# Optimization experiments

Measured on AMD Instinct MI355X. Metric: run time of the kernel, lower is better.

Reference implementation:

```python
import jax, jax.numpy as jnp
import numpy as np

NUM_CAPS_OUT = 10
NUM_NODES = 32 * 6 * 6  # 1152
IN_DIM = 8
OUT_DIM = 16
ROUTING_ITERS = 3


def squash(x):
    # scale = |x|^2/(1+|x|^2); out = scale * x/|x|  (no epsilon, faithful to torch)
    sn = jnp.sum(x * x, axis=-1, keepdims=True)
    return sn / (1.0 + sn) * x / jnp.sqrt(sn)


def setup_inputs() -> dict:
    key = jax.random.key(0)
    ks = jax.random.split(key, 6)
    B = 512
    images = jax.random.normal(ks[0], (B, 1, 28, 28), dtype=jnp.float32)
    # ConvLayer: Conv2d(1, 256, k=9, s=1) with bias
    conv1_w = jax.random.normal(ks[1], (256, 1, 9, 9), dtype=jnp.float32) * 0.05
    conv1_b = jnp.zeros((256,), dtype=jnp.float32)
    prim_w = jax.random.normal(ks[2], (8 * 32, 256, 9, 9), dtype=jnp.float32) * 0.01
    prim_b = jnp.zeros((8 * 32,), dtype=jnp.float32)
    # DigitCaps weight: torch.randn(10, 1152, 8, 16)
    W = jax.random.normal(ks[3], (NUM_CAPS_OUT, NUM_NODES, IN_DIM, OUT_DIM), dtype=jnp.float32)
    return {"images": images, "conv1_w": conv1_w, "conv1_b": conv1_b,
            "prim_w": prim_w, "prim_b": prim_b, "W": W}


def reference(images, conv1_w, conv1_b, prim_w, prim_b, W):
    B = images.shape[0]
    dn = ('NCHW', 'OIHW', 'NCHW')
    # ConvLayer: 28x28 -> 20x20, 256 channels, ReLU
    x = jax.lax.conv_general_dilated(images, conv1_w, (1, 1), 'VALID', dimension_numbers=dn)
    x = jax.nn.relu(x + conv1_b[None, :, None, None])  # [B,256,20,20]
    # PrimaryCaps: 8 stacked convs -> [B, 8*32, 6, 6]; each capsule viewed as (32*6*6,)
    u = jax.lax.conv_general_dilated(x, prim_w, (2, 2), 'VALID', dimension_numbers=dn)
    u = u + prim_b[None, :, None, None]
    u = u.reshape(B, 8, NUM_NODES).transpose(0, 2, 1)  # [B,1152,8]
    u = squash(u)
    # DigitCaps: u_hat[c,b,n,o] = sum_i u[b,n,i] * W[c,n,i,o]
    u_hat = jnp.einsum('bni,cnio->cbno', u, W)  # [10,B,1152,16]
    # Dynamic routing (3 iterations). b_ij kept as [...,1]: torch replicates it
    # across the 16 out dims identically, so math is unchanged.
    b_ij = jnp.zeros(u_hat.shape[:-1] + (1,), dtype=u_hat.dtype)
    v_j = None
    for it in range(ROUTING_ITERS):
        c_ij = jax.nn.softmax(b_ij, axis=2)            # softmax over nodes
        s_j = jnp.sum(c_ij * u_hat, axis=2, keepdims=True)  # [10,B,1,16]
        v_j = squash(s_j)
        if it < ROUTING_ITERS - 1:
            a_ij = jnp.sum(u_hat * v_j, axis=-1, keepdims=True)  # [10,B,1152,1]
            b_ij = b_ij + a_ij
    # squeeze -> [10,B,16], transpose(0,1) -> [B,10,16]
    return v_j[:, :, 0, :].transpose(1, 0, 2)
```

## Files before the change

### kernel.cpp

```cpp
#include <hip/hip_runtime.h>
#include <hip/hip_bf16.h>
#include <cstddef>
#include <cstdint>

typedef __attribute__((ext_vector_type(8))) short v8s;
typedef __attribute__((ext_vector_type(16))) float v16f;

#define GLDS(SRC, DST) __builtin_amdgcn_global_load_lds( \
    (const __attribute__((address_space(1))) void*)(SRC), \
    (__attribute__((address_space(3))) void*)(DST), 16, 0, 0)

#define WAIT_VM4() asm volatile("s_waitcnt vmcnt(4)" ::: "memory")
#define WAIT_VM0() asm volatile("s_waitcnt vmcnt(0)" ::: "memory")
#define SCHED0()   __builtin_amdgcn_sched_barrier(0)

__device__ __forceinline__ void bf16split(float x, unsigned short& h, unsigned short& l) {
    union { float f; unsigned u; } a; a.f = x;
    unsigned r = a.u + 0x7fff + ((a.u >> 16) & 1);
    h = (unsigned short)(r >> 16);
    union { unsigned u; float f; } hb; hb.u = (unsigned)h << 16;
    union { float f; unsigned u; } b; b.f = x - hb.f;
    unsigned r2 = b.u + 0x7fff + ((b.u >> 16) & 1);
    l = (unsigned short)(r2 >> 16);
}

__global__ __launch_bounds__(256) void prep_kernel(
    const float* __restrict__ cw, const float* __restrict__ pw,
    float* __restrict__ wT1, char* __restrict__ wpk)
{
    int idx = blockIdx.x * 256 + threadIdx.x;
    if (idx < 81 * 256) {
        int k = idx >> 8, oc = idx & 255;
        wT1[idx] = cw[oc * 81 + k];
    }
    int Q = idx & 2047;
    int slab = idx >> 11;
    int D = Q << 4;
    int R = D >> 9;
    int v = (D & 511) ^ ((R & 31) << 4);
    int h = v >> 7, pl = (v >> 6) & 1, icb = v & 63;
    int ch = h * 64 + R;
    int g = slab / 81, k = slab - g * 81;
    int ic0 = g * 32 + (icb >> 1);
    const float* src = pw + ((size_t)ch * 256 + ic0) * 81 + k;
    v8s ov;
#pragma unroll
    for (int j = 0; j < 8; ++j) {
        unsigned short hh, ll; bf16split(src[(size_t)j * 81], hh, ll);
        ov[j] = (short)(pl ? ll : hh);
    }
    *(v8s*)(wpk + (size_t)slab * 32768 + D) = ov;
}

__global__ __launch_bounds__(256) void conv1_kernel(
    const float* __restrict__ img,
    const float* __restrict__ wT1,
    const float* __restrict__ bias,
    char* __restrict__ xc2,
    int b0)
{
    const int bl = blockIdx.x;
    const int oc = threadIdx.x;
    __shared__ __align__(16) float im[784];
    const float* ib = img + (size_t)(b0 + bl) * 784;
    for (int e = oc; e < 784; e += 256) im[e] = ib[e];
    float w[81];
#pragma unroll
    for (int k = 0; k < 81; ++k) w[k] = wT1[k * 256 + oc];
    float bv = bias[oc];
    __syncthreads();
    char* ob = xc2 + (size_t)bl * 409600;
    for (int oy = 0; oy < 20; ++oy) {
        float a[20];
#pragma unroll
        for (int ox = 0; ox < 20; ++ox) a[ox] = bv;
        for (int ky = 0; ky < 9; ++ky) {
            const float* rp = &im[(oy + ky) * 28];
            float r[28];
#pragma unroll
            for (int q = 0; q < 7; ++q) {
                float4 v4 = *(const float4*)(rp + q * 4);
                r[q * 4] = v4.x; r[q * 4 + 1] = v4.y;
                r[q * 4 + 2] = v4.z; r[q * 4 + 3] = v4.w;
            }
#pragma unroll
            for (int kx = 0; kx < 9; ++kx) {
                float wv = w[ky * 9 + kx];
#pragma unroll
                for (int ox = 0; ox < 20; ++ox)
                    a[ox] = fmaf(wv, r[ox + kx], a[ox]);
            }
        }
#pragma unroll
        for (int ox = 0; ox < 20; ++ox) {
            float av = fmaxf(a[ox], 0.f);
            unsigned short h, l; bf16split(av, h, l);
            char* rp2 = ob + (size_t)(oy * 20 + ox) * 1024;
            *(unsigned short*)(rp2 + oc * 2) = h;
            *(unsigned short*)(rp2 + 512 + oc * 2) = l;
        }
    }
}

__global__ __launch_bounds__(512, 1) void gemm_kernel(
    const char* __restrict__ xc2,
    const char* __restrict__ wpk,
    float* __restrict__ prim,
    int M, int Mtiles, int gm0)
{
    __shared__ __align__(128) char As[2][24576];
    __shared__ __align__(128) char Bs[3][32768];
    const int tid = threadIdx.x;
    const int w = tid >> 6, lane = tid & 63;
    const int wm = w & 1, wn = w >> 1;
    const int col = lane & 31, kg = lane >> 5;
    const int id = blockIdx.x;
    const int g = id / Mtiles;
    const int tile = id - g * Mtiles;
    const int m0 = tile * 192;

    int pbase[3], asrc[3];
#pragma unroll
    for (int i = 0; i < 3; ++i) {
        int d = (w * 3 + i) * 1024 + lane * 16;
        int R = d >> 9;
        int v = (d & 511) ^ ((R & 31) << 4);
        int h = v >> 7, pl = (v >> 6) & 1, icb = v & 63;
        int m = m0 + 48 * h + R; if (m >= M) m = M - 1;
        int b = m / 36, s6 = m - b * 36;
        pbase[i] = b * 400 + (s6 / 6) * 40 + (s6 % 6) * 2;
        asrc[i] = pl * 512 + g * 64 + icb;
    }
    int Abase[3], Ahof[3], Axor[3];
#pragma unroll
    for (int fm = 0; fm < 3; ++fm) {
        int m = wm * 96 + fm * 32 + col;
        int h = m / 48, R = m - h * 48;
        Abase[fm] = R * 512;
        Ahof[fm] = h * 128;
        Axor[fm] = (R & 31) << 4;
    }
    const char* wg = wpk + (size_t)g * 81 * 32768;

    v16f acc[3][2];
#pragma unroll
    for (int i = 0; i < 3; ++i)
#pragma unroll
        for (int j = 0; j < 2; ++j)
#pragma unroll
            for (int e = 0; e < 16; ++e) acc[i][j][e] = 0.f;

    auto gldsA = [&](int nb, int kk, int i) {
        const int koff = (kk / 9) * 20 + (kk % 9);
        GLDS(xc2 + (size_t)(pbase[i] + koff) * 1024 + asrc[i],
             &As[nb][(w * 3 + i) * 1024]);
    };
    auto gldsB = [&](int nb, int kk, int i) {
        GLDS(wg + (size_t)kk * 32768 + (w * 4 + i) * 1024 + lane * 16,
             &Bs[nb][(w * 4 + i) * 1024]);
    };

#pragma unroll
    for (int i = 0; i < 3; ++i) gldsA(0, 0, i);
#pragma unroll
    for (int i = 0; i < 4; ++i) gldsB(0, 0, i);
#pragma unroll
    for (int i = 0; i < 4; ++i) gldsB(1, 1, i);
    WAIT_VM4(); SCHED0();
    __builtin_amdgcn_s_barrier(); SCHED0();

    const int xr = col << 4;
    for (int k = 0; k < 81; ++k) {
        const char* Ab = &As[k & 1][0];
        const char* Bb = &Bs[k % 3][0];
        const int nA = (k + 1) & 1, nB = (k + 2) % 3;
        const bool stA = (k < 80), stB = (k < 79);

#pragma unroll
        for (int s = 0; s < 2; ++s) {
            const int vb = s * 32 + kg * 16;
            v8s Ah[3], Al[3], Bh[2], Bl[2];
#pragma unroll
            for (int fm = 0; fm < 3; ++fm) {
                const char* ap = Ab + Abase[fm];
                Ah[fm] = *(const v8s*)(ap + ((Ahof[fm] + vb) ^ Axor[fm]));
                Al[fm] = *(const v8s*)(ap + ((Ahof[fm] + 64 + vb) ^ Axor[fm]));
            }
#pragma unroll
            for (int fn = 0; fn < 2; ++fn) {
                const char* bp = Bb + (fn * 32 + col) * 512;
                Bh[fn] = *(const v8s*)(bp + ((wn * 128 + vb) ^ xr));
                Bl[fn] = *(const v8s*)(bp + ((wn * 128 + 64 + vb) ^ xr));
            }
            if (s == 0) {
                if (stA) { gldsA(nA, k + 1, 0); gldsA(nA, k + 1, 1); gldsA(nA, k + 1, 2); }
                if (stB) gldsB(nB, k + 2, 0);
            } else {
                if (stB) { gldsB(nB, k + 2, 1); gldsB(nB, k + 2, 2); gldsB(nB, k + 2, 3); }
            }

            __builtin_amdgcn_s_barrier();
            SCHED0();
            __builtin_amdgcn_s_setprio(1);
#pragma unroll
            for (int fn = 0; fn < 2; ++fn)
#pragma unroll
                for (int fm = 0; fm < 3; ++fm) {
                    acc[fm][fn] = __builtin_amdgcn_mfma_f32_32x32x16_bf16(Al[fm], Bh[fn], acc[fm][fn], 0, 0, 0);
                    acc[fm][fn] = __builtin_amdgcn_mfma_f32_32x32x16_bf16(Ah[fm], Bl[fn], acc[fm][fn], 0, 0, 0);
                    acc[fm][fn] = __builtin_amdgcn_mfma_f32_32x32x16_bf16(Ah[fm], Bh[fn], acc[fm][fn], 0, 0, 0);
                }
            __builtin_amdgcn_s_setprio(0);
            SCHED0();
            if (s == 0) {
                __builtin_amdgcn_s_barrier();
            } else if (stA) {
                if (stB) { WAIT_VM4(); } else { WAIT_VM0(); }
                SCHED0();
                __builtin_amdgcn_s_barrier(); SCHED0();
            }
        }
    }

    float* pg = prim + (size_t)gm0 * 256;
#pragma unroll
    for (int fm = 0; fm < 3; ++fm)
#pragma unroll
        for (int fn = 0; fn < 2; ++fn) {
            int ch = wn * 64 + fn * 32 + col;
#pragma unroll
            for (int rg = 0; rg < 16; ++rg) {
                int row = (rg & 3) + 8 * (rg >> 2) + 4 * kg;
                int m = m0 + wm * 96 + fm * 32 + row;
                if (m < M) atomicAdd(&pg[(size_t)m * 256 + ch], acc[fm][fn][rg]);
            }
        }
}

__global__ __launch_bounds__(256) void prim2u_kernel(
    const float* __restrict__ prim, const float* __restrict__ pb,
    float* __restrict__ u, int M)
{
    __shared__ float p[64 * 257];
    __shared__ float bsh[256];
    const int tid = threadIdx.x;
    const int rows0 = blockIdx.x * 64;
    bsh[tid] = pb[tid];
#pragma unroll
    for (int j = 0; j < 16; ++j) {
        int e4 = j * 256 + tid;
        int row = e4 >> 6, c4 = (e4 & 63) << 2;
        int rr = rows0 + row; if (rr >= M) rr = M - 1;
        float4 a = *(const float4*)(prim + (size_t)rr * 256 + c4);
        float* pp = &p[row * 257 + c4];
        pp[0] = a.x; pp[1] = a.y; pp[2] = a.z; pp[3] = a.w;
    }
    __syncthreads();
#pragma unroll
    for (int j = 0; j < 8; ++j) {
        int idx = j * 256 + tid;
        int row = idx & 63, cc = idx >> 6;
        int m = rows0 + row;
        if (m >= M) continue;
        int b = m / 36, s = m - b * 36;
        float p8[8]; float sn = 0.f;
#pragma unroll
        for (int d = 0; d < 8; ++d) {
            float v = p[row * 257 + d * 32 + cc] + bsh[d * 32 + cc];
            p8[d] = v; sn += v * v;
        }
        float fac = sqrtf(sn) / (1.0f + sn);
        float4 o0, o1;
        o0.x = fac * p8[0]; o0.y = fac * p8[1]; o0.z = fac * p8[2]; o0.w = fac * p8[3];
        o1.x = fac * p8[4]; o1.y = fac * p8[5]; o1.z = fac * p8[6]; o1.w = fac * p8[7];
        float* up = u + ((size_t)b * 1152 + cc * 36 + s) * 8;
        *(float4*)up = o0;
        *(float4*)(up + 4) = o1;
    }
}

__global__ __launch_bounds__(512) void routing_kernel(
    const float* __restrict__ u,
    const float* __restrict__ W,
    float* __restrict__ out,
    int B, int npairs)
{
    const int id = blockIdx.x;
    const int c = id / npairs;
    const int pair = id - c * npairs;
    const int b0 = pair * 2;
    const int tid = threadIdx.x;
    __shared__ float uht[2][16][1152];
    __shared__ float bijs[2][1152];
    __shared__ float red[2][4 * 17];
    __shared__ float sred[2][17];
    __shared__ float mred[2][4];

    const float* __restrict__ Wc = W + (size_t)c * (1152 * 128);
    const int b1 = (b0 + 1 < B) ? b0 + 1 : b0;
    const float* __restrict__ ub0 = u + (size_t)b0 * 9216;
    const float* __restrict__ ub1 = u + (size_t)b1 * 9216;

    for (int n = tid; n < 1152; n += 512) {
        const float4* p0 = (const float4*)(ub0 + n * 8);
        const float4* p1 = (const float4*)(ub1 + n * 8);
        float4 a0 = p0[0], a1 = p0[1], c0 = p1[0], c1 = p1[1];
        float uu0[8] = {a0.x, a0.y, a0.z, a0.w, a1.x, a1.y, a1.z, a1.w};
        float uu1[8] = {c0.x, c0.y, c0.z, c0.w, c1.x, c1.y, c1.z, c1.w};
        float acc0[16], acc1[16];
#pragma unroll
        for (int o = 0; o < 16; ++o) { acc0[o] = 0.f; acc1[o] = 0.f; }
        const float* wn = Wc + n * 128;
#pragma unroll
        for (int i = 0; i < 8; ++i)
#pragma unroll
            for (int o = 0; o < 16; ++o) {
                float wv = wn[i * 16 + o];
                acc0[o] = fmaf(uu0[i], wv, acc0[o]);
                acc1[o] = fmaf(uu1[i], wv, acc1[o]);
            }
#pragma unroll
        for (int o = 0; o < 16; ++o) { uht[0][o][n] = acc0[o]; uht[1][o][n] = acc1[o]; }
        bijs[0][n] = 0.f; bijs[1][n] = 0.f;
    }
    __syncthreads();

    const int img = tid >> 8, t = tid & 255;
    const int wid = t >> 6, lane = t & 63;
    const float* __restrict__ UHT = &uht[img][0][0];
    float* __restrict__ bij = bijs[img];
    float* __restrict__ redi = red[img];
    float* __restrict__ sredi = sred[img];
    float* __restrict__ mredi = mred[img];

    float fac = 0.f, inv = 0.f;
    for (int it = 0; it < 3; ++it) {
        float m = -3.4e38f;
        for (int n = t; n < 1152; n += 256) m = fmaxf(m, bij[n]);
#pragma unroll
        for (int off = 32; off > 0; off >>= 1) m = fmaxf(m, __shfl_down(m, off));
        if (lane == 0) mredi[wid] = m;
        __syncthreads();
        float M = fmaxf(fmaxf(mredi[0], mredi[1]), fmaxf(mredi[2], mredi[3]));
        float se = 0.f;
        float sp[16];
#pragma unroll
        for (int o = 0; o < 16; ++o) sp[o] = 0.f;
        for (int n = t; n < 1152; n += 256) {
            float e = expf(bij[n] - M);
            se += e;
#pragma unroll
            for (int o = 0; o < 16; ++o) sp[o] = fmaf(e, UHT[o * 1152 + n], sp[o]);
        }
#pragma unroll
        for (int o = 0; o < 16; ++o)
#pragma unroll
            for (int off = 32; off > 0; off >>= 1) sp[o] += __shfl_down(sp[o], off);
#pragma unroll
        for (int off = 32; off > 0; off >>= 1) se += __shfl_down(se, off);
        if (lane == 0) {
#pragma unroll
            for (int o = 0; o < 16; ++o) redi[wid * 17 + o] = sp[o];
            redi[wid * 17 + 16] = se;
        }
        __syncthreads();
        if (t < 17)
            sredi[t] = redi[t] + redi[17 + t] + redi[34 + t] + redi[51 + t];
        __syncthreads();
        inv = 1.0f / sredi[16];
        float sn = 0.f;
        float sj[16];
#pragma unroll
        for (int o = 0; o < 16; ++o) { sj[o] = sredi[o] * inv; sn = fmaf(sj[o], sj[o], sn); }
        fac = sqrtf(sn) / (1.0f + sn);
        if (it < 2) {
            float v[16];
#pragma unroll
            for (int o = 0; o < 16; ++o) v[o] = fac * sj[o];
            for (int n = t; n < 1152; n += 256) {
                float a = 0.f;
#pragma unroll
                for (int o = 0; o < 16; ++o) a = fmaf(UHT[o * 1152 + n], v[o], a);
                bij[n] += a;
            }
        }
        __syncthreads();
    }
    if (t < 16 && b0 + img < B)
        out[((size_t)(b0 + img) * 10 + c) * 16 + t] = fac * (sredi[t] * inv);
}

extern "C" void kernel_launch(void* const* d_in, const int* in_sizes, int n_in,
                              void* d_out, int out_size, void* d_ws, size_t ws_size,
                              hipStream_t stream) {
    const float* images  = (const float*)d_in[0];
    const float* conv1_w = (const float*)d_in[1];
    const float* conv1_b = (const float*)d_in[2];
    const float* prim_w  = (const float*)d_in[3];
    const float* prim_b  = (const float*)d_in[4];
    const float* W       = (const float*)d_in[5];
    float* out = (float*)d_out;

    const int B = in_sizes[0] / 784;
    const int Mg = B * 36;
    const size_t usz = (size_t)B * 1152 * 8 * 4;
    const size_t xc2_full = (size_t)B * 409600;

    char* wsb = (char*)d_ws;
    size_t off = 0;
    float* wT1 = (float*)(wsb + off);
    off += 81 * 256 * 4;
    off = (off + 1023) & ~(size_t)1023;
    char* wpk = wsb + off;
    off += (size_t)648 * 32768;
    float* prim = (float*)(wsb + off);
    off += (size_t)Mg * 256 * 4;
    size_t rem = (ws_size > off) ? ws_size - off : 0;

    float* u;
    char* xc2base;
    int Bc;
    if (rem >= xc2_full) {
        xc2base = wsb + off;
        u = (float*)xc2base;
        Bc = B;
    } else {
        u = (float*)(wsb + off);
        off += usz;
        rem = (ws_size > off) ? ws_size - off : 0;
        xc2base = wsb + off;
        long Bcmax = (long)(rem / 409600);
        if (Bcmax < 1) Bcmax = 1;
        if (Bcmax > B) Bcmax = B;
        int nch = (int)((B + Bcmax - 1) / Bcmax);
        Bc = (B + nch - 1) / nch;
        Bc = (Bc + 15) & ~15;
        if (Bc > Bcmax) Bc = (int)(Bcmax & ~15L);
        if (Bc < 1) Bc = (int)Bcmax;
    }

    hipMemsetAsync(prim, 0, (size_t)Mg * 256 * 4, stream);
    prep_kernel<<<5184, 256, 0, stream>>>(conv1_w, prim_w, wT1, wpk);

    for (int b0 = 0; b0 < B; b0 += Bc) {
        int bc = (B - b0 < Bc) ? (B - b0) : Bc;
        conv1_kernel<<<bc, 256, 0, stream>>>(images, wT1, conv1_b, xc2base, b0);
        int M = bc * 36;
        int Mtiles = (M + 191) / 192;
        gemm_kernel<<<Mtiles * 8, 512, 0, stream>>>(xc2base, wpk, prim, M, Mtiles, b0 * 36);
    }
    prim2u_kernel<<<(Mg + 63) / 64, 256, 0, stream>>>(prim, prim_b, u, Mg);
    int npairs = (B + 1) / 2;
    routing_kernel<<<npairs * 10, 512, 0, stream>>>(u, W, out, B, npairs);
}
```

Baseline: 972.8 us.

## Keep routing u_hat in registers, one image per 256-thread block

The routing kernel now keeps each thread's u_hat rows (5 nodes × 16 outputs) and routing logits in registers instead of a large shared-memory buffer covering two images per block. Blocks become one image with 256 threads, and W loads are vectorised as float4. This removes heavy LDS use so more blocks can run per CU and LDS traffic in the routing loops disappears. In exchange, W is re-read per image rather than shared across a pair, and register pressure rises.

```diff
diff --git a/kernel.cpp b/kernel.cpp
--- a/kernel.cpp
+++ b/kernel.cpp
@@ -279,79 +279,77 @@
     }
 }
 
-__global__ __launch_bounds__(512) void routing_kernel(
+__global__ __launch_bounds__(256) void routing_kernel(
     const float* __restrict__ u,
     const float* __restrict__ W,
     float* __restrict__ out,
-    int B, int npairs)
+    int B)
 {
     const int id = blockIdx.x;
-    const int c = id / npairs;
-    const int pair = id - c * npairs;
-    const int b0 = pair * 2;
-    const int tid = threadIdx.x;
-    __shared__ float uht[2][16][1152];
-    __shared__ float bijs[2][1152];
-    __shared__ float red[2][4 * 17];
-    __shared__ float sred[2][17];
-    __shared__ float mred[2][4];
+    const int c = id / B;
+    const int b = id - c * B;
+    const int t = threadIdx.x;
+    const int wid = t >> 6, lane = t & 63;
+    __shared__ float red[4 * 17];
+    __shared__ float sred[17];
+    __shared__ float mred[4];
 
     const float* __restrict__ Wc = W + (size_t)c * (1152 * 128);
-    const int b1 = (b0 + 1 < B) ? b0 + 1 : b0;
-    const float* __restrict__ ub0 = u + (size_t)b0 * 9216;
-    const float* __restrict__ ub1 = u + (size_t)b1 * 9216;
-
-    for (int n = tid; n < 1152; n += 512) {
-        const float4* p0 = (const float4*)(ub0 + n * 8);
-        const float4* p1 = (const float4*)(ub1 + n * 8);
-        float4 a0 = p0[0], a1 = p0[1], c0 = p1[0], c1 = p1[1];
-        float uu0[8] = {a0.x, a0.y, a0.z, a0.w, a1.x, a1.y, a1.z, a1.w};
-        float uu1[8] = {c0.x, c0.y, c0.z, c0.w, c1.x, c1.y, c1.z, c1.w};
-        float acc0[16], acc1[16];
-#pragma unroll
-        for (int o = 0; o < 16; ++o) { acc0[o] = 0.f; acc1[o] = 0.f; }
-        const float* wn = Wc + n * 128;
-#pragma unroll
-        for (int i = 0; i < 8; ++i)
-#pragma unroll
-            for (int o = 0; o < 16; ++o) {
-                float wv = wn[i * 16 + o];
-                acc0[o] = fmaf(uu0[i], wv, acc0[o]);
-                acc1[o] = fmaf(uu1[i], wv, acc1[o]);
-            }
-#pragma unroll
-        for (int o = 0; o < 16; ++o) { uht[0][o][n] = acc0[o]; uht[1][o][n] = acc1[o]; }
-        bijs[0][n] = 0.f; bijs[1][n] = 0.f;
-    }
-    __syncthreads();
-
-    const int img = tid >> 8, t = tid & 255;
-    const int wid = t >> 6, lane = t & 63;
-    const float* __restrict__ UHT = &uht[img][0][0];
-    float* __restrict__ bij = bijs[img];
-    float* __restrict__ redi = red[img];
-    float* __restrict__ sredi = sred[img];
-    float* __restrict__ mredi = mred[img];
+    const float* __restrict__ ub = u + (size_t)b * 9216;
+
+    float uh[5][16];
+    float bij[5];
+#pragma unroll
+    for (int j = 0; j < 5; ++j) {
+        const int n = t + 256 * j;
+        const bool valid = (j < 4) || (t < 128);
+#pragma unroll
+        for (int o = 0; o < 16; ++o) uh[j][o] = 0.f;
+        if (valid) {
+            const float4* up = (const float4*)(ub + n * 8);
+            float4 a0 = up[0], a1 = up[1];
+            float uu[8] = {a0.x, a0.y, a0.z, a0.w, a1.x, a1.y, a1.z, a1.w};
+            const float4* w4 = (const float4*)(Wc + (size_t)n * 128);
+#pragma unroll
+            for (int i = 0; i < 8; ++i)
+#pragma unroll
+                for (int q = 0; q < 4; ++q) {
+                    float4 wv = w4[i * 4 + q];
+                    uh[j][q * 4 + 0] = fmaf(uu[i], wv.x, uh[j][q * 4 + 0]);
+                    uh[j][q * 4 + 1] = fmaf(uu[i], wv.y, uh[j][q * 4 + 1]);
+                    uh[j][q * 4 + 2] = fmaf(uu[i], wv.z, uh[j][q * 4 + 2]);
+                    uh[j][q * 4 + 3] = fmaf(uu[i], wv.w, uh[j][q * 4 + 3]);
+                }
+            bij[j] = 0.f;
+        } else {
+            bij[j] = -3.4e38f;
+        }
+    }
 
     float fac = 0.f, inv = 0.f;
     for (int it = 0; it < 3; ++it) {
-        float m = -3.4e38f;
-        for (int n = t; n < 1152; n += 256) m = fmaxf(m, bij[n]);
+        float m = bij[0];
+#pragma unroll
+        for (int j = 1; j < 5; ++j) m = fmaxf(m, bij[j]);
 #pragma unroll
         for (int off = 32; off > 0; off >>= 1) m = fmaxf(m, __shfl_down(m, off));
-        if (lane == 0) mredi[wid] = m;
+        if (lane == 0) mred[wid] = m;
         __syncthreads();
-        float M = fmaxf(fmaxf(mredi[0], mredi[1]), fmaxf(mredi[2], mredi[3]));
+        float M = fmaxf(fmaxf(mred[0], mred[1]), fmaxf(mred[2], mred[3]));
         float se = 0.f;
+        float ee[5];
         float sp[16];
 #pragma unroll
         for (int o = 0; o < 16; ++o) sp[o] = 0.f;
-        for (int n = t; n < 1152; n += 256) {
-            float e = expf(bij[n] - M);
+#pragma unroll
+        for (int j = 0; j < 5; ++j) {
+            float e = expf(bij[j] - M);
+            ee[j] = e;
             se += e;
 #pragma unroll
-            for (int o = 0; o < 16; ++o) sp[o] = fmaf(e, UHT[o * 1152 + n], sp[o]);
-        }
+            for (int o = 0; o < 16; ++o) sp[o] = fmaf(e, uh[j][o], sp[o]);
+        }
+        (void)ee;
 #pragma unroll
         for (int o = 0; o < 16; ++o)
 #pragma unroll
@@ -360,34 +358,34 @@
         for (int off = 32; off > 0; off >>= 1) se += __shfl_down(se, off);
         if (lane == 0) {
 #pragma unroll
-            for (int o = 0; o < 16; ++o) redi[wid * 17 + o] = sp[o];
-            redi[wid * 17 + 16] = se;
+            for (int o = 0; o < 16; ++o) red[wid * 17 + o] = sp[o];
+            red[wid * 17 + 16] = se;
         }
         __syncthreads();
         if (t < 17)
-            sredi[t] = redi[t] + redi[17 + t] + redi[34 + t] + redi[51 + t];
+            sred[t] = red[t] + red[17 + t] + red[34 + t] + red[51 + t];
         __syncthreads();
-        inv = 1.0f / sredi[16];
+        inv = 1.0f / sred[16];
         float sn = 0.f;
         float sj[16];
 #pragma unroll
-        for (int o = 0; o < 16; ++o) { sj[o] = sredi[o] * inv; sn = fmaf(sj[o], sj[o], sn); }
+        for (int o = 0; o < 16; ++o) { sj[o] = sred[o] * inv; sn = fmaf(sj[o], sj[o], sn); }
         fac = sqrtf(sn) / (1.0f + sn);
         if (it < 2) {
             float v[16];
 #pragma unroll
             for (int o = 0; o < 16; ++o) v[o] = fac * sj[o];
-            for (int n = t; n < 1152; n += 256) {
+#pragma unroll
+            for (int j = 0; j < 5; ++j) {
                 float a = 0.f;
 #pragma unroll
-                for (int o = 0; o < 16; ++o) a = fmaf(UHT[o * 1152 + n], v[o], a);
-                bij[n] += a;
+                for (int o = 0; o < 16; ++o) a = fmaf(uh[j][o], v[o], a);
+                bij[j] += a;
             }
         }
         __syncthreads();
     }
-    if (t < 16 && b0 + img < B)
-        out[((size_t)(b0 + img) * 10 + c) * 16 + t] = fac * (sredi[t] * inv);
+    if (t < 16) out[((size_t)b * 10 + c) * 16 + t] = fac * (sred[t] * inv);
 }
 
 extern "C" void kernel_launch(void* const* d_in, const int* in_sizes, int n_in,
@@ -450,6 +448,5 @@
         gemm_kernel<<<Mtiles * 8, 512, 0, stream>>>(xc2base, wpk, prim, M, Mtiles, b0 * 36);
     }
     prim2u_kernel<<<(Mg + 63) / 64, 256, 0, stream>>>(prim, prim_b, u, Mg);
-    int npairs = (B + 1) / 2;
-    routing_kernel<<<npairs * 10, 512, 0, stream>>>(u, W, out, B, npairs);
-}
+    routing_kernel<<<B * 10, 256, 0, stream>>>(u, W, out, B);
+}
```

Result: slower. 1.333 ms (+37.0%).
